# Kernel optimization log

Hardware: AMD Instinct MI355X
Metric: run time of the kernel (lower is better)

## Reference

```python
import jax, jax.numpy as jnp
import numpy as np

N, D, H, E = 16384, 1024, 4096, 8

def setup_inputs() -> dict:
    key = jax.random.key(0)
    ks = jax.random.split(key, 7)
    s = 0.02
    return {
        "x": jax.random.normal(ks[0], (N, D), dtype=jnp.float32),
        "Ws": jax.random.normal(ks[1], (H, D), dtype=jnp.float32) * s,
        "bs": jax.random.normal(ks[2], (H,), dtype=jnp.float32) * s,
        "We": jax.random.normal(ks[3], (E, H, D), dtype=jnp.float32) * s,
        "be": jax.random.normal(ks[4], (E, H), dtype=jnp.float32) * s,
        "Wr": jax.random.normal(ks[5], (E, D), dtype=jnp.float32) * s,
        "br": jax.random.normal(ks[6], (E,), dtype=jnp.float32) * s,
    }

def reference(x, Ws, bs, We, be, Wr, br):
    # shared FFN: [N, H]
    shared = x @ Ws.T + bs
    # router: softmax over experts, top-1 via argmax (argmax(softmax)==argmax(logits), kept faithful)
    expert_scores = jax.nn.softmax(x @ Wr.T + br, axis=-1)  # [N, E]
    token_expert = jnp.argmax(expert_scores, axis=-1)       # [N]
    # mask-accumulate over the small fixed expert set (dense per-expert FFN as in source)
    routed = jnp.zeros_like(shared)
    num_experts = We.shape[0]
    for i in range(num_experts):
        mask = (token_expert == i).astype(shared.dtype)[:, None]  # [N, 1]
        routed = routed + mask * (x @ We[i].T + be[i])
    return shared + routed
```

## Files before the change

### kernel.cpp

```cpp
#include <hip/hip_runtime.h>
#include <stdint.h>

#define N_TOK 16384
#define DDIM  1024
#define HDIM  4096
#define NEXP  8
#define BM    256
#define MAXMT 72
#define MAXNR 5

typedef __attribute__((ext_vector_type(8))) short short8;
typedef __attribute__((ext_vector_type(4))) float f32x4;

__device__ __forceinline__ unsigned short f2b(float f) {
    union { float f; unsigned int u; } x; x.f = f;
    unsigned int r = x.u + 0x7FFFu + ((x.u >> 16) & 1u);
    return (unsigned short)(r >> 16);
}

__global__ __launch_bounds__(256)
void k_router_cast(const float* __restrict__ x, const float* __restrict__ Wr,
                   const float* __restrict__ br, unsigned short* __restrict__ xb,
                   int* __restrict__ eid)
{
    __shared__ float wr[NEXP * DDIM];
    const int t = threadIdx.x;
    for (int i = t; i < NEXP * DDIM / 4; i += 256)
        ((float4*)wr)[i] = ((const float4*)Wr)[i];
    __syncthreads();
    const int lane = t & 63;
    const int n = blockIdx.x * 4 + (t >> 6);
    const float* xr = x + (size_t)n * DDIM;
    double acc[NEXP];
#pragma unroll
    for (int e = 0; e < NEXP; ++e) acc[e] = 0.0;
#pragma unroll
    for (int j = 0; j < 4; ++j) {
        const int d = j * 256 + lane * 4;
        float4 v = *(const float4*)(xr + d);
        unsigned long long pk =
            (unsigned long long)(f2b(v.x) | ((unsigned int)f2b(v.y) << 16)) |
            ((unsigned long long)(f2b(v.z) | ((unsigned int)f2b(v.w) << 16)) << 32);
        *(unsigned long long*)(xb + (size_t)n * DDIM + d) = pk;
#pragma unroll
        for (int e = 0; e < NEXP; ++e) {
            const float* w = wr + e * DDIM + d;
            acc[e] += (double)v.x * (double)w[0];
            acc[e] += (double)v.y * (double)w[1];
            acc[e] += (double)v.z * (double)w[2];
            acc[e] += (double)v.w * (double)w[3];
        }
    }
#pragma unroll
    for (int e = 0; e < NEXP; ++e)
#pragma unroll
        for (int off = 32; off > 0; off >>= 1)
            acc[e] += __shfl_down(acc[e], off);
    if (lane == 0) {
        double best = acc[0] + (double)br[0];
        int bi = 0;
#pragma unroll
        for (int e = 1; e < NEXP; ++e) {
            double v = acc[e] + (double)br[e];
            if (v > best) { best = v; bi = e; }
        }
        eid[n] = bi;
    }
}

__global__ __launch_bounds__(256)
void k_hist(const int* __restrict__ eid, int* __restrict__ counts)
{
    __shared__ int h[NEXP];
    const int t = threadIdx.x;
    if (t < NEXP) h[t] = 0;
    __syncthreads();
    atomicAdd(&h[eid[blockIdx.x * 256 + t]], 1);
    __syncthreads();
    if (t < NEXP && h[t]) atomicAdd(&counts[t * 16], h[t]);
}

__global__ void k_scan(const int* __restrict__ counts, int* __restrict__ texp,
                       int* __restrict__ pbase)
{
    if (threadIdx.x == 0) {
        int tt = 0;
        for (int e = 0; e < NEXP; ++e) {
            pbase[e] = tt * BM;
            const int nt = (counts[e * 16] + BM - 1) / BM;
            for (int i = 0; i < nt; ++i) texp[tt++] = e;
        }
        pbase[8] = tt;
        for (; tt < MAXMT; ++tt) texp[tt] = -1;
    }
}

__global__ __launch_bounds__(256)
void k_scatter(const int* __restrict__ eid, const int* __restrict__ pbase,
               int* __restrict__ cursors, int* __restrict__ perm)
{
    __shared__ int h[NEXP];
    __shared__ int base[NEXP];
    const int t = threadIdx.x;
    if (t < NEXP) h[t] = 0;
    __syncthreads();
    const int n = blockIdx.x * 256 + t;
    const int e = eid[n];
    const int rank = atomicAdd(&h[e], 1);
    __syncthreads();
    if (t < NEXP) base[t] = h[t] ? atomicAdd(&cursors[t * 16], h[t]) : 0;
    __syncthreads();
    perm[pbase[e] + base[e] + rank] = n;
}

__global__ __launch_bounds__(256)
void k_combine_w(const float* __restrict__ Ws, const float* __restrict__ We,
                 unsigned short* __restrict__ wc)
{
    const size_t i = ((size_t)blockIdx.x * 256 + threadIdx.x) * 8;
    const size_t hd = i & (size_t)(HDIM * DDIM - 1);
    float4 a0 = *(const float4*)(We + i);
    float4 a1 = *(const float4*)(We + i + 4);
    float4 b0 = *(const float4*)(Ws + hd);
    float4 b1 = *(const float4*)(Ws + hd + 4);
    uint4 o;
    o.x = f2b(a0.x + b0.x) | ((unsigned)f2b(a0.y + b0.y) << 16);
    o.y = f2b(a0.z + b0.z) | ((unsigned)f2b(a0.w + b0.w) << 16);
    o.z = f2b(a1.x + b1.x) | ((unsigned)f2b(a1.y + b1.y) << 16);
    o.w = f2b(a1.z + b1.z) | ((unsigned)f2b(a1.w + b1.w) << 16);
    *(uint4*)(wc + i) = o;
}

__global__ __launch_bounds__(256)
void k_combine_b(const float* __restrict__ bs, const float* __restrict__ be,
                 float* __restrict__ bc)
{
    const int i = blockIdx.x * 256 + threadIdx.x;
    bc[i] = bs[i & (HDIM - 1)] + be[i];
}

#define SBAR()   __builtin_amdgcn_s_barrier()
#define SCHED0() __builtin_amdgcn_sched_barrier(0)
#define LGKM0()  asm volatile("s_waitcnt lgkmcnt(0)" ::: "memory")

__global__ __launch_bounds__(512, 2)
void k_gemm(const unsigned short* __restrict__ X, const unsigned short* __restrict__ W,
            const float* __restrict__ bc, const int* __restrict__ perm,
            const int* __restrict__ texp, const int* __restrict__ realM_p,
            float* __restrict__ out)
{
    __shared__ unsigned short lds[65536];
    __shared__ int   toksLDS[MAXNR][256];
    __shared__ float biasLDS[MAXNR][256];

    const int realM = realM_p[8];
    const int base  = blockIdx.x;
    const int tnr   = base & 15;
    const int tmB   = base >> 4;
    const int nR    = (realM - tmB + 15) >> 4;
    const int T     = nR << 4;

    const int t    = threadIdx.x;
    const int lane = t & 63;
    const int wid  = t >> 6;
    const int wm   = wid >> 2;
    const int wn   = wid & 3;

    const int srow    = t >> 3;
    const int schunkE = (((t & 7) ^ (srow & 7)) << 3);
    unsigned short* dstT = lds + (t << 3);

    const int rA   = lane & 15;
    const int c0   = ((lane >> 4) << 3) ^ ((lane & 7) << 3);
    const int c1   = c0 ^ 32;
    const int aBase = ((2 + wm) << 13) + (rA << 6);
    const int bBase = ((wn >> 1) << 13) + ((wn & 1) << 12) + (rA << 6);
    const int colBase = tnr * 256 + wn * 64 + rA;

    int ePk = 0;
#pragma unroll
    for (int w = 0; w < MAXNR; ++w) {
        const int ev = (w < nR) ? texp[tmB + (w << 4)] : 0;
        ePk |= (ev & 15) << (w << 2);
    }
    if (t < 256) {
#pragma unroll
        for (int w = 0; w < MAXNR; ++w) {
            if (w < nR) {
                toksLDS[w][t] = perm[(tmB + (w << 4)) * 256 + t];
                const int ev = (ePk >> (w << 2)) & 15;
                biasLDS[w][t] = bc[ev * HDIM + tnr * 256 + t];
            }
        }
    }
    __syncthreads();

    int tokCur[4], tokNext[4];
#pragma unroll
    for (int i = 0; i < 4; ++i) {
        int a = toksLDS[0][i * 64 + srow];
        tokCur[i] = a < 0 ? 0 : a;
        int b = (nR > 1) ? toksLDS[1][i * 64 + srow] : 0;
        tokNext[i] = b < 0 ? 0 : b;
    }

    f32x4 acc[8][4];
    {
        float bn[4];
#pragma unroll
        for (int n = 0; n < 4; ++n) bn[n] = biasLDS[0][wn * 64 + n * 16 + rA];
#pragma unroll
        for (int m = 0; m < 8; ++m)
#pragma unroll
            for (int n = 0; n < 4; ++n)
                acc[m][n] = (f32x4){bn[n], bn[n], bn[n], bn[n]};
    }
    short8 fa[8][2], fb[4][2];

    auto STAGE = [&](int sg, int tau) {
        if (sg >= (nR << 6)) return;
        const int tloc = sg >> 2;
        const int h    = sg & 3;
        const int kb   = (tloc & 15) << 6;
        unsigned short* d = dstT + ((tloc & 1) << 15) + (h << 13);
        const unsigned short *s0, *s1;
        if (h < 2) {
            const int wS = tloc >> 4;
            const int ee = (ePk >> (wS << 2)) & 15;
            const size_t r0 = (size_t)(ee * HDIM + tnr * 256 + h * 128 + srow) * DDIM
                              + schunkE + kb;
            s0 = W + r0; s1 = W + r0 + (size_t)64 * DDIM;
        } else {
            const bool nxt = (tloc >> 4) != (tau >> 4);
            const int i0 = (h - 2) << 1;
            const int ta = nxt ? tokNext[i0]     : tokCur[i0];
            const int tb = nxt ? tokNext[i0 + 1] : tokCur[i0 + 1];
            s0 = X + (size_t)ta * DDIM + schunkE + kb;
            s1 = X + (size_t)tb * DDIM + schunkE + kb;
        }
        __builtin_amdgcn_global_load_lds(
            (const __attribute__((address_space(1))) void*)s0,
            (__attribute__((address_space(3))) void*)d, 16, 0, 0);
        __builtin_amdgcn_global_load_lds(
            (const __attribute__((address_space(1))) void*)s1,
            (__attribute__((address_space(3))) void*)(d + 4096), 16, 0, 0);
    };

#define LDA(m) \
    fa[m][0] = *(const short8*)&lds[bufOff + aBase + (m)*1024 + c0]; \
    fa[m][1] = *(const short8*)&lds[bufOff + aBase + (m)*1024 + c1];
#define LDB(n) \
    fb[n][0] = *(const short8*)&lds[bufOff + bBase + (n)*1024 + c0]; \
    fb[n][1] = *(const short8*)&lds[bufOff + bBase + (n)*1024 + c1];
#define MM(m,n) \
    acc[m][n] = __builtin_amdgcn_mfma_f32_16x16x32_bf16(fa[m][0], fb[n][0], acc[m][n], 0,0,0); \
    acc[m][n] = __builtin_amdgcn_mfma_f32_16x16x32_bf16(fa[m][1], fb[n][1], acc[m][n], 0,0,0);

#pragma unroll
    for (int s = 0; s < 7; ++s) STAGE(s, 0);
    asm volatile("s_waitcnt vmcnt(6)" ::: "memory");
    SCHED0(); SBAR(); SCHED0();

    int w = 0;
#pragma unroll 1
    for (int tau = 0; tau < T; ++tau) {
        const int tt = tau & 15;
        const int bufOff = (tau & 1) << 15;
        const int sig = (tau << 2) + 7;

        LDB(0) LDB(1) LDA(0) LDA(1)
        STAGE(sig, tau);
        SCHED0(); SBAR(); LGKM0(); SCHED0();
        __builtin_amdgcn_s_setprio(1);
        if (tt != 0) { MM(6,2) MM(6,3) MM(7,2) MM(7,3) }
        MM(0,0) MM(0,1) MM(1,0) MM(1,1)
        __builtin_amdgcn_s_setprio(0);
        SCHED0(); SBAR(); SCHED0();
        LDB(2) LDB(3) LDA(2) LDA(3)
        STAGE(sig + 1, tau);
        SCHED0(); SBAR(); LGKM0(); SCHED0();
        __builtin_amdgcn_s_setprio(1);
        MM(0,2) MM(0,3) MM(1,2) MM(1,3) MM(2,0) MM(2,1) MM(3,0) MM(3,1)
        __builtin_amdgcn_s_setprio(0);
        SCHED0(); SBAR(); SCHED0();
        LDA(4) LDA(5) LDA(6) LDA(7)
        STAGE(sig + 2, tau);
        SCHED0(); SBAR(); LGKM0(); SCHED0();
        __builtin_amdgcn_s_setprio(1);
        MM(2,2) MM(2,3) MM(3,2) MM(3,3) MM(4,0) MM(4,1) MM(5,0) MM(5,1)
        __builtin_amdgcn_s_setprio(0);
        SCHED0(); SBAR(); SCHED0();
        STAGE(sig + 3, tau);
        SCHED0(); SBAR(); SCHED0();
        __builtin_amdgcn_s_setprio(1);
        MM(4,2) MM(4,3) MM(5,2) MM(5,3) MM(6,0) MM(6,1) MM(7,0) MM(7,1)
        if (tt == 15) { MM(6,2) MM(6,3) MM(7,2) MM(7,3) }
        __builtin_amdgcn_s_setprio(0);
        SCHED0();
        if (tau < T - 2)       { asm volatile("s_waitcnt vmcnt(6)" ::: "memory"); }
        else if (tau == T - 2) { asm volatile("s_waitcnt vmcnt(0)" ::: "memory"); }
        SBAR(); SCHED0();

        if (tt == 15) {
            const int rsub = (lane >> 4) * 4;
#pragma unroll
            for (int m = 0; m < 8; ++m) {
                const int rl = wm * 128 + m * 16 + rsub;
                int tk[4];
#pragma unroll
                for (int j = 0; j < 4; ++j) tk[j] = toksLDS[w][rl + j];
#pragma unroll
                for (int n = 0; n < 4; ++n) {
                    const int col = colBase + n * 16;
#pragma unroll
                    for (int j = 0; j < 4; ++j)
                        if (tk[j] >= 0) out[(size_t)tk[j] * HDIM + col] = acc[m][n][j];
                }
            }
            if (w + 1 < nR) {
                float bn[4];
#pragma unroll
                for (int n = 0; n < 4; ++n) bn[n] = biasLDS[w + 1][wn * 64 + n * 16 + rA];
#pragma unroll
                for (int m = 0; m < 8; ++m)
#pragma unroll
                    for (int n = 0; n < 4; ++n)
                        acc[m][n] = (f32x4){bn[n], bn[n], bn[n], bn[n]};
#pragma unroll
                for (int i = 0; i < 4; ++i) tokCur[i] = tokNext[i];
                if (w + 2 < nR) {
#pragma unroll
                    for (int i = 0; i < 4; ++i) {
                        int v = toksLDS[w + 2][i * 64 + srow];
                        tokNext[i] = v < 0 ? 0 : v;
                    }
                }
            }
            ++w;
        }
    }
#undef LDA
#undef LDB
#undef MM
}

extern "C" void kernel_launch(void* const* d_in, const int* in_sizes, int n_in,
                              void* d_out, int out_size, void* d_ws, size_t ws_size,
                              hipStream_t stream)
{
    const float* x  = (const float*)d_in[0];
    const float* Ws = (const float*)d_in[1];
    const float* bs = (const float*)d_in[2];
    const float* We = (const float*)d_in[3];
    const float* be = (const float*)d_in[4];
    const float* Wr = (const float*)d_in[5];
    const float* br = (const float*)d_in[6];
    float* out = (float*)d_out;
    char* ws = (char*)d_ws;

    unsigned short* xb  = (unsigned short*)(ws + 0);
    unsigned short* wc  = (unsigned short*)(ws + 33554432);
    float*          bc  = (float*)(ws + 100663296);
    int*            eid = (int*)(ws + 100794368);
    int*            perm= (int*)(ws + 100859904);
    int*            cnt = (int*)(ws + 100933632);
    int*            cur = (int*)(ws + 100934144);
    int*            pb  = (int*)(ws + 100934656);
    int*            texp= (int*)(ws + 100934720);

    hipMemsetAsync(perm, 0xFF, MAXMT * BM * sizeof(int), stream);
    hipMemsetAsync(cnt, 0, 1024, stream);

    k_router_cast<<<N_TOK / 4, 256, 0, stream>>>(x, Wr, br, xb, eid);
    k_combine_w<<<(NEXP * (size_t)HDIM * DDIM / 8) / 256, 256, 0, stream>>>(Ws, We, wc);
    k_combine_b<<<NEXP * HDIM / 256, 256, 0, stream>>>(bs, be, bc);
    k_hist<<<N_TOK / 256, 256, 0, stream>>>(eid, cnt);
    k_scan<<<1, 64, 0, stream>>>(cnt, texp, pb);
    k_scatter<<<N_TOK / 256, 256, 0, stream>>>(eid, pb, cur, perm);
    k_gemm<<<256, 512, 0, stream>>>(xb, wc, bc, perm, texp, pb, out);
}
```

Before: 292.4 us.

## Issue all LDS fragment loads upfront and replace barriers with lgkmcnt waits

Restructures the main GEMM k-loop so all A and B fragment loads for the tile are issued at the start, and MFMA groups are gated by partial lgkmcnt waits instead of a barrier and full LDS wait per quarter. Global staging for three of the four stages is moved after the LDS reads complete, and the cross-iteration deferred MM(6/7,2/3) trick is removed. This cuts the workgroup barriers per iteration from five to two and lets the LDS reads overlap with the MFMAs. In exchange it raises register pressure, and the hand-counted lgkmcnt values must match the real number of outstanding LDS ops.

Measured after the change: 283.3 us. 3.1% less time.

```diff
diff --git a/kernel.cpp b/kernel.cpp
--- a/kernel.cpp
+++ b/kernel.cpp
@@ -268,35 +268,28 @@
         const int bufOff = (tau & 1) << 15;
         const int sig = (tau << 2) + 7;
 
-        LDB(0) LDB(1) LDA(0) LDA(1)
+        LDB(0) LDB(1) LDB(2) LDB(3) LDA(0) LDA(1)
+        SCHED0();
+        LDA(2) LDA(3)
+        SCHED0();
+        LDA(4) LDA(5) LDA(6) LDA(7)
         STAGE(sig, tau);
-        SCHED0(); SBAR(); LGKM0(); SCHED0();
+        SCHED0();
+        asm volatile("s_waitcnt lgkmcnt(12)" ::: "memory"); SCHED0();
         __builtin_amdgcn_s_setprio(1);
-        if (tt != 0) { MM(6,2) MM(6,3) MM(7,2) MM(7,3) }
-        MM(0,0) MM(0,1) MM(1,0) MM(1,1)
-        __builtin_amdgcn_s_setprio(0);
-        SCHED0(); SBAR(); SCHED0();
-        LDB(2) LDB(3) LDA(2) LDA(3)
-        STAGE(sig + 1, tau);
-        SCHED0(); SBAR(); LGKM0(); SCHED0();
+        MM(0,0) MM(0,1) MM(0,2) MM(0,3) MM(1,0) MM(1,1) MM(1,2) MM(1,3)
+        __builtin_amdgcn_s_setprio(0); SCHED0();
+        asm volatile("s_waitcnt lgkmcnt(8)" ::: "memory"); SCHED0();
         __builtin_amdgcn_s_setprio(1);
-        MM(0,2) MM(0,3) MM(1,2) MM(1,3) MM(2,0) MM(2,1) MM(3,0) MM(3,1)
-        __builtin_amdgcn_s_setprio(0);
-        SCHED0(); SBAR(); SCHED0();
-        LDA(4) LDA(5) LDA(6) LDA(7)
-        STAGE(sig + 2, tau);
-        SCHED0(); SBAR(); LGKM0(); SCHED0();
+        MM(2,0) MM(2,1) MM(2,2) MM(2,3) MM(3,0) MM(3,1) MM(3,2) MM(3,3)
+        __builtin_amdgcn_s_setprio(0); SCHED0();
+        LGKM0(); SBAR(); SCHED0();
+        STAGE(sig + 1, tau); STAGE(sig + 2, tau); STAGE(sig + 3, tau);
+        SCHED0();
         __builtin_amdgcn_s_setprio(1);
-        MM(2,2) MM(2,3) MM(3,2) MM(3,3) MM(4,0) MM(4,1) MM(5,0) MM(5,1)
-        __builtin_amdgcn_s_setprio(0);
-        SCHED0(); SBAR(); SCHED0();
-        STAGE(sig + 3, tau);
-        SCHED0(); SBAR(); SCHED0();
-        __builtin_amdgcn_s_setprio(1);
-        MM(4,2) MM(4,3) MM(5,2) MM(5,3) MM(6,0) MM(6,1) MM(7,0) MM(7,1)
-        if (tt == 15) { MM(6,2) MM(6,3) MM(7,2) MM(7,3) }
-        __builtin_amdgcn_s_setprio(0);
-        SCHED0();
+        MM(4,0) MM(4,1) MM(4,2) MM(4,3) MM(5,0) MM(5,1) MM(5,2) MM(5,3)
+        MM(6,0) MM(6,1) MM(6,2) MM(6,3) MM(7,0) MM(7,1) MM(7,2) MM(7,3)
+        __builtin_amdgcn_s_setprio(0); SCHED0();
         if (tau < T - 2)       { asm volatile("s_waitcnt vmcnt(6)" ::: "memory"); }
         else if (tau == T - 2) { asm volatile("s_waitcnt vmcnt(0)" ::: "memory"); }
         SBAR(); SCHED0();
```
